# Optimization experiments

Hardware: AMD Instinct MI355X
Metric: run time of the kernel (lower is better)

Reference implementation:

```python
import jax, jax.numpy as jnp
import numpy as np

B, T, DIM = 2, 2048, 1024
HID = 4096
H, KVH, HD = 16, 4, 64
WIN = 512
NORM_EPS = 1e-5
QK_EPS = 1e-6
LS_INIT = 0.01


def setup_inputs() -> dict:
    key = jax.random.key(0)
    ks = jax.random.split(key, 12)
    s = lambda fan_in: 1.0 / np.sqrt(fan_in)
    return {
        "x": jax.random.normal(ks[0], (B, T, DIM), jnp.float32),
        # torch Linear weights are (out, in); y = x @ W.T
        "wq": jax.random.normal(ks[1], (H * HD, DIM), jnp.float32) * s(DIM),
        "wk": jax.random.normal(ks[2], (KVH * HD, DIM), jnp.float32) * s(DIM),
        "wv": jax.random.normal(ks[3], (KVH * HD, DIM), jnp.float32) * s(DIM),
        "wo": jax.random.normal(ks[4], (DIM, H * HD), jnp.float32) * s(H * HD),
        "w1": jax.random.normal(ks[5], (HID, DIM), jnp.float32) * s(DIM),
        "w2": jax.random.normal(ks[6], (DIM, HID), jnp.float32) * s(HID),
        "w3": jax.random.normal(ks[7], (HID, DIM), jnp.float32) * s(DIM),
        "q_norm_w": jnp.ones((HD,), jnp.float32),
        "k_norm_w": jnp.ones((HD,), jnp.float32),
        "attn_norm_w": jnp.ones((DIM,), jnp.float32),
        "ffn_norm_w": jnp.ones((DIM,), jnp.float32),
        "attn_scale": jnp.full((DIM,), LS_INIT, jnp.float32),
        "ffn_scale": jnp.full((DIM,), LS_INIT, jnp.float32),
    }


def _rmsnorm(x, w, eps):
    return x * jax.lax.rsqrt(jnp.mean(x * x, axis=-1, keepdims=True) + eps) * w


def _attention(x, wq, wk, wv, wo, q_norm_w, k_norm_w):
    b, t, _ = x.shape
    q = (x @ wq.T).reshape(b, t, H, HD)
    k = (x @ wk.T).reshape(b, t, KVH, HD)
    v = (x @ wv.T).reshape(b, t, KVH, HD)
    q = _rmsnorm(q, q_norm_w, QK_EPS)
    k = _rmsnorm(k, k_norm_w, QK_EPS)
    # GQA: repeat kv heads to H heads
    rep = H // KVH
    k = jnp.repeat(k, rep, axis=2)  # (b,t,H,HD)
    v = jnp.repeat(v, rep, axis=2)
    scale = 1.0 / np.sqrt(HD)
    scores = jnp.einsum("bqhd,bkhd->bhqk", q, k) * scale  # (b,H,t,t)
    row = jnp.arange(t)[:, None]
    col = jnp.arange(t)[None, :]
    mask = (row >= col) & (row - col < WIN)  # (t,t) bool
    scores = jnp.where(mask[None, None], scores, -jnp.inf)
    probs = jax.nn.softmax(scores, axis=-1)
    y = jnp.einsum("bhqk,bkhd->bqhd", probs, v).reshape(b, t, H * HD)
    return y @ wo.T


def reference(x, wq, wk, wv, wo, w1, w2, w3, q_norm_w, k_norm_w,
              attn_norm_w, ffn_norm_w, attn_scale, ffn_scale):
    r = _attention(_rmsnorm(x, attn_norm_w, NORM_EPS), wq, wk, wv, wo,
                   q_norm_w, k_norm_w)
    h = x + r * attn_scale
    hn = _rmsnorm(h, ffn_norm_w, NORM_EPS)
    ffn = (jax.nn.silu(hn @ w1.T) * (hn @ w3.T)) @ w2.T
    return h + ffn * ffn_scale
```

## Files before the change

### kernel.cpp

```cpp
#include <hip/hip_runtime.h>

typedef unsigned short u16;
typedef unsigned int u32;
typedef unsigned char u8;
typedef short bf16x8 __attribute__((ext_vector_type(8)));
typedef float f32x4 __attribute__((ext_vector_type(4)));
typedef float f32x16 __attribute__((ext_vector_type(16)));
typedef int i32x4 __attribute__((ext_vector_type(4)));
typedef int i32x8 __attribute__((ext_vector_type(8)));

#define AS1 __attribute__((address_space(1)))
#define AS3 __attribute__((address_space(3)))

#define B_ 2
#define T_ 2048
#define DIM_ 1024
#define HID_ 4096
#define H_ 16
#define KVH_ 4
#define HD_ 64
#define WIN_ 512

#define SCALE_A 0x7C7C7C7C
#define SCALE_B 0x79797979

__device__ __forceinline__ u16 f2bf(float f) {
    union { float f; u32 u; } v; v.f = f;
    u32 r = v.u + 0x7FFFu + ((v.u >> 16) & 1u);
    return (u16)(r >> 16);
}
__device__ __forceinline__ float bf2f(u32 u) {
    union { u32 u; float f; } v; v.u = u << 16;
    return v.f;
}
__device__ __forceinline__ float4 ld4bf(const u16* p) {
    uint2 u = *(const uint2*)p;
    float4 r;
    r.x = bf2f(u.x & 0xFFFFu); r.y = bf2f(u.x >> 16);
    r.z = bf2f(u.y & 0xFFFFu); r.w = bf2f(u.y >> 16);
    return r;
}
__device__ __forceinline__ void load_lds16(const void* g, void* l) {
    __builtin_amdgcn_global_load_lds((AS1 void*)(g), (AS3 void*)(l), 16, 0, 0);
}
#define WAITBAR(N) asm volatile("s_waitcnt vmcnt(" #N ")\n\ts_barrier" ::: "memory")

__global__ __launch_bounds__(256) void mega_cvt(const float* __restrict__ wq,
                                                const float* __restrict__ wk,
                                                const float* __restrict__ wv,
                                                const float* __restrict__ wo,
                                                const float* __restrict__ w1,
                                                const float* __restrict__ w3,
                                                const float* __restrict__ w2,
                                                u16* __restrict__ wqkv,
                                                u16* __restrict__ wo_b,
                                                u8* __restrict__ w13_8,
                                                u8* __restrict__ w2_8) {
    int i = blockIdx.x * 256 + threadIdx.x;
    if (i < 655360) {
        const float* s; uint2* dbase; size_t didx;
        if (i < 262144)      { s = wq + (size_t)i * 4; dbase = (uint2*)wqkv; didx = i; }
        else if (i < 327680) { int f = i - 262144; s = wk + (size_t)f * 4; dbase = (uint2*)wqkv; didx = 262144 + f; }
        else if (i < 393216) { int f = i - 327680; s = wv + (size_t)f * 4; dbase = (uint2*)wqkv; didx = 327680 + f; }
        else                 { int f = i - 393216; s = wo + (size_t)f * 4; dbase = (uint2*)wo_b; didx = f; }
        float4 v = *(const float4*)s;
        u32 lo = (u32)f2bf(v.x) | ((u32)f2bf(v.y) << 16);
        u32 hi = (u32)f2bf(v.z) | ((u32)f2bf(v.w) << 16);
        dbase[didx] = make_uint2(lo, hi);
    } else {
        const float* s; u32* dbase; size_t didx;
        if (i < 1703936)      { int f = i - 655360;  int c = f >> 8; int n = (c >> 5) * 64 + (c & 31);
                                s = w1 + (size_t)f * 4; dbase = (u32*)w13_8; didx = (size_t)n * 256 + (f & 255); }
        else if (i < 2752512) { int f = i - 1703936; int c = f >> 8; int n = (c >> 5) * 64 + 32 + (c & 31);
                                s = w3 + (size_t)f * 4; dbase = (u32*)w13_8; didx = (size_t)n * 256 + (f & 255); }
        else                  { int f = i - 2752512; s = w2 + (size_t)f * 4; dbase = (u32*)w2_8; didx = f; }
        float4 v = *(const float4*)s;
        int p = __builtin_amdgcn_cvt_pk_fp8_f32(v.x * 64.f, v.y * 64.f, 0, false);
        p = __builtin_amdgcn_cvt_pk_fp8_f32(v.z * 64.f, v.w * 64.f, p, true);
        dbase[didx] = (u32)p;
    }
}

__global__ __launch_bounds__(256) void rmsnorm_kernel(const float* __restrict__ x,
                                                      const float* __restrict__ w,
                                                      u16* __restrict__ out, float eps) {
    int row = blockIdx.x, tid = threadIdx.x;
    const float4 v = ((const float4*)(x + (size_t)row * DIM_))[tid];
    float ss = v.x * v.x + v.y * v.y + v.z * v.z + v.w * v.w;
#pragma unroll
    for (int m = 1; m < 64; m <<= 1) ss += __shfl_xor(ss, m);
    __shared__ float part[4];
    if ((tid & 63) == 0) part[tid >> 6] = ss;
    __syncthreads();
    float tot = part[0] + part[1] + part[2] + part[3];
    float r = rsqrtf(tot * (1.0f / DIM_) + eps);
    const float4 wv = ((const float4*)w)[tid];
    u32 lo = (u32)f2bf(v.x * r * wv.x) | ((u32)f2bf(v.y * r * wv.y) << 16);
    u32 hi = (u32)f2bf(v.z * r * wv.z) | ((u32)f2bf(v.w * r * wv.w) << 16);
    ((uint2*)(out + (size_t)row * DIM_))[tid] = make_uint2(lo, hi);
}

__global__ __launch_bounds__(256) void fuse_attn_kernel(const float* __restrict__ x,
                                                        const u16* __restrict__ p,
                                                        const float* __restrict__ ascale,
                                                        const float* __restrict__ fnw,
                                                        float* __restrict__ h,
                                                        u8* __restrict__ xn8) {
    int row = blockIdx.x, tid = threadIdx.x;
    const float4 xv = ((const float4*)(x + (size_t)row * DIM_))[tid];
    float4 a0 = ld4bf(p + (size_t)row * DIM_ + tid * 4);
    float4 a1 = ld4bf(p + 4194304 + (size_t)row * DIM_ + tid * 4);
    const float4 sc = ((const float4*)ascale)[tid];
    float4 hv;
    hv.x = xv.x + (a0.x + a1.x) * sc.x;
    hv.y = xv.y + (a0.y + a1.y) * sc.y;
    hv.z = xv.z + (a0.z + a1.z) * sc.z;
    hv.w = xv.w + (a0.w + a1.w) * sc.w;
    ((float4*)(h + (size_t)row * DIM_))[tid] = hv;
    float ss = hv.x * hv.x + hv.y * hv.y + hv.z * hv.z + hv.w * hv.w;
#pragma unroll
    for (int m = 1; m < 64; m <<= 1) ss += __shfl_xor(ss, m);
    __shared__ float part[4];
    if ((tid & 63) == 0) part[tid >> 6] = ss;
    __syncthreads();
    float tot = part[0] + part[1] + part[2] + part[3];
    float r = rsqrtf(tot * (1.0f / DIM_) + 1e-5f) * 8.0f;
    const float4 wv = ((const float4*)fnw)[tid];
    int pk = __builtin_amdgcn_cvt_pk_fp8_f32(hv.x * r * wv.x, hv.y * r * wv.y, 0, false);
    pk = __builtin_amdgcn_cvt_pk_fp8_f32(hv.z * r * wv.z, hv.w * r * wv.w, pk, true);
    ((u32*)xn8)[(size_t)row * 256 + tid] = (u32)pk;
}

__global__ __launch_bounds__(256) void fuse_ffn_kernel(const float* __restrict__ h,
                                                       const u16* __restrict__ p,
                                                       const float* __restrict__ fscale,
                                                       float* __restrict__ out) {
    int row = blockIdx.x, tid = threadIdx.x;
    const float4 hv = ((const float4*)(h + (size_t)row * DIM_))[tid];
    size_t off = (size_t)row * DIM_ + tid * 4;
    float4 a0 = ld4bf(p + off);
    float4 a1 = ld4bf(p + 4194304 + off);
    float4 a2 = ld4bf(p + 8388608 + off);
    float4 a3 = ld4bf(p + 12582912 + off);
    const float4 sc = ((const float4*)fscale)[tid];
    float4 o;
    o.x = hv.x + (a0.x + a1.x + a2.x + a3.x) * sc.x;
    o.y = hv.y + (a0.y + a1.y + a2.y + a3.y) * sc.y;
    o.z = hv.z + (a0.z + a1.z + a2.z + a3.z) * sc.z;
    o.w = hv.w + (a0.w + a1.w + a2.w + a3.w) * sc.w;
    ((float4*)(out + (size_t)row * DIM_))[tid] = o;
}

__global__ __launch_bounds__(256) void qkv_post_kernel(const u16* __restrict__ qkv,
                                                       const float* __restrict__ qw,
                                                       const float* __restrict__ kw,
                                                       u16* __restrict__ Qb,
                                                       u16* __restrict__ Kb,
                                                       u16* __restrict__ Vb) {
    int bt = blockIdx.x;
    int b = bt >> 11, t = bt & (T_ - 1);
    int wave = threadIdx.x >> 6, lane = threadIdx.x & 63;
    const u16* row0 = qkv + (size_t)bt * 1536;
    const u16* row1 = row0 + 6291456;
    float qwl = qw[lane], kwl = kw[lane];
#pragma unroll
    for (int i = 0; i < 4; i++) {
        int h = wave * 4 + i;
        float v = bf2f(row0[h * 64 + lane]) + bf2f(row1[h * 64 + lane]);
        float ss = v * v;
#pragma unroll
        for (int m = 1; m < 64; m <<= 1) ss += __shfl_xor(ss, m);
        float r = rsqrtf(ss * (1.0f / 64.0f) + 1e-6f);
        Qb[(((size_t)(b * H_ + h)) * T_ + t) * HD_ + lane] = f2bf(v * r * qwl);
    }
    {
        float v = bf2f(row0[1024 + wave * 64 + lane]) + bf2f(row1[1024 + wave * 64 + lane]);
        float ss = v * v;
#pragma unroll
        for (int m = 1; m < 64; m <<= 1) ss += __shfl_xor(ss, m);
        float r = rsqrtf(ss * (1.0f / 64.0f) + 1e-6f);
        Kb[(((size_t)(b * KVH_ + wave)) * T_ + t) * HD_ + lane] = f2bf(v * r * kwl);
        float vv = bf2f(row0[1280 + wave * 64 + lane]) + bf2f(row1[1280 + wave * 64 + lane]);
        Vb[(((size_t)(b * KVH_ + wave)) * T_ + t) * HD_ + lane] = f2bf(vv);
    }
}

__global__ __launch_bounds__(256) void vtrans_kernel(const u16* __restrict__ Vb,
                                                     u16* __restrict__ Vt) {
    const int bk = blockIdx.x >> 5;
    const int t0 = (blockIdx.x & 31) * 64;
    const int tid = threadIdx.x;
    __shared__ __align__(16) u16 tile[64][64];
    const u16* src = Vb + ((size_t)bk * T_ + t0) * HD_;
#pragma unroll
    for (int i = 0; i < 2; i++) {
        int g = tid + i * 256;
        int r = g >> 3, c8 = g & 7;
        *(bf16x8*)&tile[r][c8 * 8] = *(const bf16x8*)(src + (size_t)r * HD_ + c8 * 8);
    }
    __syncthreads();
    const int d = tid >> 2, ts = (tid & 3) * 16;
    u16 buf[16];
#pragma unroll
    for (int j = 0; j < 16; j++) buf[j] = tile[ts + j][d];
    u16* dst = Vt + (size_t)bk * HD_ * T_ + (size_t)d * T_ + t0 + ts;
    *(bf16x8*)(dst) = *(const bf16x8*)&buf[0];
    *(bf16x8*)(dst + 8) = *(const bf16x8*)&buf[8];
}

__global__ __launch_bounds__(512, 2) void flash_kernel(const u16* __restrict__ Qb,
                                                       const u16* __restrict__ Kb,
                                                       const u16* __restrict__ Vt,
                                                       u16* __restrict__ Ob) {
    const int b = blockIdx.z, kvh = blockIdx.y, qt = blockIdx.x;
    const int q0 = qt * 64;
    const int tid = threadIdx.x, wave = tid >> 6, lane = tid & 63;
    const int head = wave & 3, qhalf = wave >> 2;
    const int h = kvh * 4 + head;
    const int m = lane & 15, quad = lane >> 4;

    __shared__ __align__(16) u16 Ks[2][4096];
    __shared__ __align__(16) u16 Vs[2][4096];
    __shared__ __align__(16) u16 Ps[8][16 * 72];

    const u16* Qp = Qb + ((size_t)(b * H_ + h) * T_) * HD_;
    const u16* Kp = Kb + ((size_t)(b * KVH_ + kvh) * T_) * HD_;
    const u16* Vp = Vt + ((size_t)(b * KVH_ + kvh) * HD_) * T_;

    const int qbase = q0 + qhalf * 32;
    bf16x8 qa[2][2];
#pragma unroll
    for (int qs = 0; qs < 2; qs++) {
        const u16* qp = Qp + (size_t)(qbase + qs * 16 + m) * 64 + quad * 8;
        qa[qs][0] = *(const bf16x8*)(qp);
        qa[qs][1] = *(const bf16x8*)(qp + 32);
    }

    f32x4 o[2][4] = {};
    float mrun[2] = {-1e30f, -1e30f}, lrun[2] = {0.f, 0.f};

    const int kt0 = (q0 >= WIN_) ? ((q0 - (WIN_ - 1)) >> 6) : 0;
    const int kt1 = qt;

    const int srow = tid >> 3;
    const int schunk = (tid & 7) ^ (srow & 7);
    const u16* Ksrc = Kp + (size_t)srow * 64 + schunk * 8;
    const u16* Vsrc = Vp + (size_t)srow * T_ + schunk * 8;
    const int ldsOff = wave * 512;

    load_lds16(Ksrc + (size_t)kt0 * 4096, &Ks[0][ldsOff]);
    load_lds16(Vsrc + kt0 * 64, &Vs[0][ldsOff]);

    for (int kt = kt0; kt <= kt1; ++kt) {
        const int kbase = kt << 6;
        const int cur = (kt - kt0) & 1;
        if (kt < kt1) {
            load_lds16(Ksrc + (size_t)(kt + 1) * 4096, &Ks[cur ^ 1][ldsOff]);
            load_lds16(Vsrc + (kt + 1) * 64, &Vs[cur ^ 1][ldsOff]);
            WAITBAR(2);
        } else {
            WAITBAR(0);
        }
        bf16x8 kf[4][2], vb[4][2];
#pragma unroll
        for (int st = 0; st < 4; st++) {
            const int r64 = (st * 16 + m) * 64;
#pragma unroll
            for (int hf = 0; hf < 2; hf++) {
                const int c = (((hf << 2) + quad) ^ (m & 7)) * 8;
                kf[st][hf] = *(const bf16x8*)&Ks[cur][r64 + c];
                vb[st][hf] = *(const bf16x8*)&Vs[cur][r64 + c];
            }
        }
#pragma unroll
        for (int qs = 0; qs < 2; qs++) {
            const int qlo_s = qbase + qs * 16;
            if (kbase <= qlo_s + 15 && kbase >= qlo_s - 574) {
                f32x4 s4[4];
#pragma unroll
                for (int st = 0; st < 4; st++) {
                    f32x4 z = {0.f, 0.f, 0.f, 0.f};
                    z = __builtin_amdgcn_mfma_f32_16x16x32_bf16(kf[st][0], qa[qs][0], z, 0, 0, 0);
                    z = __builtin_amdgcn_mfma_f32_16x16x32_bf16(kf[st][1], qa[qs][1], z, 0, 0, 0);
                    s4[st] = z;
                }
                float v[16];
                const bool full = (kbase + 63 <= qlo_s) && (kbase >= qlo_s - 496);
                if (full) {
#pragma unroll
                    for (int i = 0; i < 16; i++) v[i] = s4[i >> 2][i & 3] * 0.125f;
                } else {
                    const int D = qlo_s + m - kbase - quad * 4;
#pragma unroll
                    for (int st = 0; st < 4; st++)
#pragma unroll
                        for (int r = 0; r < 4; r++) {
                            int diff = D - st * 16 - r;
                            v[st * 4 + r] = ((u32)diff < (u32)WIN_) ? s4[st][r] * 0.125f : -INFINITY;
                        }
                }
                float t0 = fmaxf(fmaxf(fmaxf(v[0], v[1]), fmaxf(v[2], v[3])),
                                 fmaxf(fmaxf(v[4], v[5]), fmaxf(v[6], v[7])));
                float t1 = fmaxf(fmaxf(fmaxf(v[8], v[9]), fmaxf(v[10], v[11])),
                                 fmaxf(fmaxf(v[12], v[13]), fmaxf(v[14], v[15])));
                float rmax = fmaxf(t0, t1);
                rmax = fmaxf(rmax, __shfl_xor(rmax, 16));
                rmax = fmaxf(rmax, __shfl_xor(rmax, 32));
                float mnew = fmaxf(mrun[qs], rmax);
                float alpha = __expf(mrun[qs] - mnew);
                float p[16];
#pragma unroll
                for (int i = 0; i < 16; i++) p[i] = __expf(v[i] - mnew);
                float u0 = ((p[0] + p[1]) + (p[2] + p[3])) + ((p[4] + p[5]) + (p[6] + p[7]));
                float u1 = ((p[8] + p[9]) + (p[10] + p[11])) + ((p[12] + p[13]) + (p[14] + p[15]));
                float psum = u0 + u1;
                psum += __shfl_xor(psum, 16);
                psum += __shfl_xor(psum, 32);
                lrun[qs] = lrun[qs] * alpha + psum;
                mrun[qs] = mnew;
#pragma unroll
                for (int d = 0; d < 4; d++) {
                    o[qs][d][0] *= alpha; o[qs][d][1] *= alpha;
                    o[qs][d][2] *= alpha; o[qs][d][3] *= alpha;
                }
#pragma unroll
                for (int st = 0; st < 4; st++) {
                    u32 lo = (u32)f2bf(p[st * 4 + 0]) | ((u32)f2bf(p[st * 4 + 1]) << 16);
                    u32 hi = (u32)f2bf(p[st * 4 + 2]) | ((u32)f2bf(p[st * 4 + 3]) << 16);
                    *(uint2*)&Ps[wave][m * 72 + st * 16 + quad * 4] = make_uint2(lo, hi);
                }
                bf16x8 pa0 = *(const bf16x8*)&Ps[wave][m * 72 + quad * 8];
                bf16x8 pa1 = *(const bf16x8*)&Ps[wave][m * 72 + 32 + quad * 8];
#pragma unroll
                for (int d = 0; d < 4; d++) {
                    o[qs][d] = __builtin_amdgcn_mfma_f32_16x16x32_bf16(vb[d][0], pa0, o[qs][d], 0, 0, 0);
                    o[qs][d] = __builtin_amdgcn_mfma_f32_16x16x32_bf16(vb[d][1], pa1, o[qs][d], 0, 0, 0);
                }
            }
        }
        asm volatile("s_barrier" ::: "memory");
    }
#pragma unroll
    for (int qs = 0; qs < 2; qs++) {
        float inv = 1.0f / lrun[qs];
        u16* ob = Ob + ((size_t)(b * T_ + qbase + qs * 16 + m)) * (H_ * HD_) + h * HD_;
#pragma unroll
        for (int d = 0; d < 4; d++) {
            u32 lo = (u32)f2bf(o[qs][d][0] * inv) | ((u32)f2bf(o[qs][d][1] * inv) << 16);
            u32 hi = (u32)f2bf(o[qs][d][2] * inv) | ((u32)f2bf(o[qs][d][3] * inv) << 16);
            *(uint2*)(ob + d * 16 + quad * 4) = make_uint2(lo, hi);
        }
    }
}

__global__ __launch_bounds__(256) void gemm_bt(const u16* __restrict__ A,
                                               const u16* __restrict__ Bt,
                                               u16* __restrict__ Cb,
                                               int M, int N, int K, int KS) {
    __shared__ __align__(16) u16 As[2][4096];
    __shared__ __align__(16) u16 Bs[2][4096];
    const int tid = threadIdx.x, wave = tid >> 6, lane = tid & 63;
    const int m = lane & 15, quad = lane >> 4;
    const int m0 = blockIdx.y * 128, n0 = blockIdx.x * 128;
    const int wm = (wave >> 1) * 64, wn = (wave & 1) * 64;
    const int kb = blockIdx.z * KS;
    const int nIter = KS >> 5;
    const int slot = wave * 2;
    const int flat0 = slot * 512 + lane * 8;
    const int row0_ = flat0 >> 5, col0 = flat0 & 31;
    const int flat1 = (slot + 1) * 512 + lane * 8;
    const int row1_ = flat1 >> 5, col1 = flat1 & 31;

    f32x4 acc[4][4] = {};

    load_lds16(A + (size_t)(m0 + row0_) * K + kb + col0, &As[0][slot * 512]);
    load_lds16(Bt + (size_t)(n0 + row0_) * K + kb + col0, &Bs[0][slot * 512]);
    load_lds16(A + (size_t)(m0 + row1_) * K + kb + col1, &As[0][(slot + 1) * 512]);
    load_lds16(Bt + (size_t)(n0 + row1_) * K + kb + col1, &Bs[0][(slot + 1) * 512]);

    for (int it = 0; it < nIter; ++it) {
        __syncthreads();
        const int cur = it & 1;
        if (it + 1 < nIter) {
            const int nb = 1 - cur;
            const int k0 = kb + (it + 1) * 32;
            load_lds16(A + (size_t)(m0 + row0_) * K + k0 + col0, &As[nb][slot * 512]);
            load_lds16(Bt + (size_t)(n0 + row0_) * K + k0 + col0, &Bs[nb][slot * 512]);
            load_lds16(A + (size_t)(m0 + row1_) * K + k0 + col1, &As[nb][(slot + 1) * 512]);
            load_lds16(Bt + (size_t)(n0 + row1_) * K + k0 + col1, &Bs[nb][(slot + 1) * 512]);
        }
        bf16x8 af[4], bfr[4];
#pragma unroll
        for (int i = 0; i < 4; i++) af[i] = *(const bf16x8*)&As[cur][(wm + i * 16 + m) * 32 + quad * 8];
#pragma unroll
        for (int j = 0; j < 4; j++) bfr[j] = *(const bf16x8*)&Bs[cur][(wn + j * 16 + m) * 32 + quad * 8];
#pragma unroll
        for (int i = 0; i < 4; i++)
#pragma unroll
            for (int j = 0; j < 4; j++)
                acc[i][j] = __builtin_amdgcn_mfma_f32_16x16x32_bf16(af[i], bfr[j], acc[i][j], 0, 0, 0);
    }

    u16* Cz = Cb + (size_t)blockIdx.z * M * N;
#pragma unroll
    for (int i = 0; i < 4; i++) {
        int rowb = m0 + wm + i * 16 + quad * 4;
#pragma unroll
        for (int j = 0; j < 4; j++) {
            int col = n0 + wn + j * 16 + m;
#pragma unroll
            for (int r = 0; r < 4; r++)
                Cz[(size_t)(rowb + r) * N + col] = f2bf(acc[i][j][r]);
        }
    }
}

#define MFMA8(a, b, c) __builtin_amdgcn_mfma_scale_f32_32x32x64_f8f6f4(a, b, c, 0, 0, 0, SCALE_A, 0, SCALE_B)
#define PHASE_MFMA(I0, I1)                           \
    __builtin_amdgcn_s_setprio(1);                   \
    acc[I0][0] = MFMA8(a0, bf0, acc[I0][0]);         \
    acc[I0][1] = MFMA8(a0, bf1, acc[I0][1]);         \
    acc[I1][0] = MFMA8(a1, bf0, acc[I1][0]);         \
    acc[I1][1] = MFMA8(a1, bf1, acc[I1][1]);         \
    __builtin_amdgcn_s_setprio(0);

template <int MODE>
__global__ __launch_bounds__(512) void gemm_fp8(const u8* __restrict__ A,
                                                const u8* __restrict__ Bt,
                                                u16* __restrict__ Cb,
                                                u8* __restrict__ C8,
                                                int M, int N, int K, int KS) {
    __shared__ __align__(16) u8 As[2][32768];
    __shared__ __align__(16) u8 Bs[2][32768];
    const int tid = threadIdx.x, wave = tid >> 6, lane = tid & 63;
    const int l31 = lane & 31, lh = lane >> 5;
    const int m0 = blockIdx.y * 256, n0 = blockIdx.x * 256;
    const int wm = (wave >> 2) * 128, wn = (wave & 3) * 64;
    const int kb = blockIdx.z * KS;
    const int KT = KS >> 7;

    const int srow = ((wave & 3) << 6) + lane;
    const u8* Asrc = A + (size_t)m0 * K + (size_t)srow * K;
    const u8* Bsrc = Bt + (size_t)n0 * K + (size_t)srow * K;
    const int wv2 = wave >> 2;
    const int ldsW = (wave & 3) << 10;

    auto STAGE = [&](const u8* src, int kk, int ks, u8* lds) {
#pragma unroll
        for (int q = 0; q < 2; q++) {
            const int ch = ks * 4 + wv2 + 2 * q;
            load_lds16(src + kk + ch * 16, lds + (ch << 12) + ldsW);
        }
    };
    auto FRAG = [&](const u8* t, int ks, int row) -> i32x8 {
        const int c0 = ks * 4 + (lh << 1);
        union { i32x4 h[2]; i32x8 v; } u;
        u.h[0] = *(const i32x4*)(t + ((c0 << 8) + row) * 16);
        u.h[1] = *(const i32x4*)(t + (((c0 + 1) << 8) + row) * 16);
        return u.v;
    };

    f32x16 acc[4][2] = {};

    STAGE(Asrc, kb, 0, As[0]);
    STAGE(Bsrc, kb, 0, Bs[0]);
    STAGE(Asrc, kb, 1, As[0]);
    STAGE(Bsrc, kb, 1, Bs[0]);

    for (int kt = 0; kt < KT - 1; ++kt) {
        const int cur = kt & 1, nb = cur ^ 1;
        const u8* Ac = As[cur];
        const u8* Bc = Bs[cur];
        const int kn = kb + (kt + 1) * 128;
        i32x8 bf0, bf1, a0, a1;
        STAGE(Asrc, kn, 0, As[nb]);
        WAITBAR(6);
        bf0 = FRAG(Bc, 0, wn + l31);
        bf1 = FRAG(Bc, 0, wn + 32 + l31);
        a0 = FRAG(Ac, 0, wm + l31);
        a1 = FRAG(Ac, 0, wm + 32 + l31);
        PHASE_MFMA(0, 1)
        STAGE(Bsrc, kn, 0, Bs[nb]);
        a0 = FRAG(Ac, 0, wm + 64 + l31);
        a1 = FRAG(Ac, 0, wm + 96 + l31);
        PHASE_MFMA(2, 3)
        STAGE(Asrc, kn, 1, As[nb]);
        WAITBAR(6);
        bf0 = FRAG(Bc, 1, wn + l31);
        bf1 = FRAG(Bc, 1, wn + 32 + l31);
        a0 = FRAG(Ac, 1, wm + l31);
        a1 = FRAG(Ac, 1, wm + 32 + l31);
        PHASE_MFMA(0, 1)
        STAGE(Bsrc, kn, 1, Bs[nb]);
        a0 = FRAG(Ac, 1, wm + 64 + l31);
        a1 = FRAG(Ac, 1, wm + 96 + l31);
        PHASE_MFMA(2, 3)
    }
    {
        const int cur = (KT - 1) & 1;
        const u8* Ac = As[cur];
        const u8* Bc = Bs[cur];
        i32x8 bf0, bf1, a0, a1;
        WAITBAR(4);
        bf0 = FRAG(Bc, 0, wn + l31);
        bf1 = FRAG(Bc, 0, wn + 32 + l31);
        a0 = FRAG(Ac, 0, wm + l31);
        a1 = FRAG(Ac, 0, wm + 32 + l31);
        PHASE_MFMA(0, 1)
        a0 = FRAG(Ac, 0, wm + 64 + l31);
        a1 = FRAG(Ac, 0, wm + 96 + l31);
        PHASE_MFMA(2, 3)
        WAITBAR(0);
        bf0 = FRAG(Bc, 1, wn + l31);
        bf1 = FRAG(Bc, 1, wn + 32 + l31);
        a0 = FRAG(Ac, 1, wm + l31);
        a1 = FRAG(Ac, 1, wm + 32 + l31);
        PHASE_MFMA(0, 1)
        a0 = FRAG(Ac, 1, wm + 64 + l31);
        a1 = FRAG(Ac, 1, wm + 96 + l31);
        PHASE_MFMA(2, 3)
    }

    if (MODE == 0) {
        u16* Cz = Cb + (size_t)blockIdx.z * M * N;
#pragma unroll
        for (int i = 0; i < 4; i++)
#pragma unroll
            for (int j = 0; j < 2; j++) {
                int col = n0 + wn + j * 32 + l31;
#pragma unroll
                for (int reg = 0; reg < 16; reg++) {
                    int row = m0 + wm + i * 32 + (reg & 3) + 8 * (reg >> 2) + 4 * lh;
                    Cz[(size_t)row * N + col] = f2bf(acc[i][j][reg]);
                }
            }
    } else {
        int c = (n0 >> 1) + (wn >> 1) + l31;
#pragma unroll
        for (int i = 0; i < 4; i++)
#pragma unroll
            for (int reg = 0; reg < 16; reg++) {
                int row = m0 + wm + i * 32 + (reg & 3) + 8 * (reg >> 2) + 4 * lh;
                float g1 = acc[i][0][reg], g3 = acc[i][1][reg];
                float res = (g1 / (1.f + __expf(-g1))) * g3 * 8.0f;
                int p = __builtin_amdgcn_cvt_pk_fp8_f32(res, res, 0, false);
                C8[(size_t)row * (N >> 1) + c] = (u8)(p & 0xFF);
            }
    }
}

extern "C" void kernel_launch(void* const* d_in, const int* in_sizes, int n_in,
                              void* d_out, int out_size, void* d_ws, size_t ws_size,
                              hipStream_t stream) {
    const float* x = (const float*)d_in[0];
    const float* wq = (const float*)d_in[1];
    const float* wk = (const float*)d_in[2];
    const float* wv = (const float*)d_in[3];
    const float* wo = (const float*)d_in[4];
    const float* w1 = (const float*)d_in[5];
    const float* w2 = (const float*)d_in[6];
    const float* w3 = (const float*)d_in[7];
    const float* qnw = (const float*)d_in[8];
    const float* knw = (const float*)d_in[9];
    const float* anw = (const float*)d_in[10];
    const float* fnw = (const float*)d_in[11];
    const float* ascale = (const float*)d_in[12];
    const float* fscale = (const float*)d_in[13];
    float* out = (float*)d_out;

    char* ws = (char*)d_ws;
    u16* wqkv_bf = (u16*)(ws + 0);
    u16* wo_bf = (u16*)(ws + 3145728);
    u8* w13_8 = (u8*)(ws + 5242880);
    u8* w2_8 = (u8*)(ws + 13631488);
    u16* xn_bf = (u16*)(ws + 17825792);
    u8* xn8 = (u8*)(ws + 26214400);
    float* h_f = (float*)(ws + 30408704);
    char* P = ws + 47185920;
    u16* qkv_part = (u16*)(P + 0);
    u16* Qb = (u16*)(P + 25165824);
    u16* Kb = (u16*)(P + 33554432);
    u16* Vb = (u16*)(P + 35651584);
    u16* att_bf = (u16*)(P + 37748736);
    u16* Vt = (u16*)(P + 46137344);
    u16* wo_part = (u16*)(P + 0);
    u8* gsw8 = (u8*)(P + 16777216);
    u16* w2_part = (u16*)(P + 33554432);

    mega_cvt<<<14848, 256, 0, stream>>>(wq, wk, wv, wo, w1, w3, w2,
                                        wqkv_bf, wo_bf, w13_8, w2_8);
    rmsnorm_kernel<<<4096, 256, 0, stream>>>(x, anw, xn_bf, 1e-5f);
    gemm_bt<<<dim3(12, 32, 2), 256, 0, stream>>>(xn_bf, wqkv_bf, qkv_part,
                                                 4096, 1536, 1024, 512);
    qkv_post_kernel<<<4096, 256, 0, stream>>>(qkv_part, qnw, knw, Qb, Kb, Vb);
    vtrans_kernel<<<256, 256, 0, stream>>>(Vb, Vt);
    flash_kernel<<<dim3(32, KVH_, B_), 512, 0, stream>>>(Qb, Kb, Vt, att_bf);
    gemm_bt<<<dim3(8, 32, 2), 256, 0, stream>>>(att_bf, wo_bf, wo_part,
                                                4096, 1024, 1024, 512);
    fuse_attn_kernel<<<4096, 256, 0, stream>>>(x, wo_part, ascale, fnw, h_f, xn8);
    gemm_fp8<1><<<dim3(32, 16, 1), 512, 0, stream>>>(xn8, w13_8, nullptr, gsw8,
                                                     4096, 8192, 1024, 1024);
    gemm_fp8<0><<<dim3(4, 16, 4), 512, 0, stream>>>(gsw8, w2_8, w2_part, nullptr,
                                                    4096, 1024, 4096, 1024);
    fuse_ffn_kernel<<<4096, 256, 0, stream>>>(h_f, w2_part, fscale, out);
}
```

Measured before the change: 319.7 us.

## Switch FP8 GEMM to 128x128 tiles with 16x16x128 scaled MFMA

Replaces the 256x256-tile, 512-thread FP8 GEMM used for the FFN projections with a 128x128-tile, 256-thread version. It uses 16x16x128 scaled MFMA instructions and a simple double-buffered loop with one barrier per k-step. Smaller tiles and less LDS per block aim to raise occupancy and grid size. In exchange it loses the hand-interleaved staging, priority hints and per-tile data reuse of the larger tile.

Result: slower. 352.6 us (+10.3%).

```diff
diff --git a/kernel.cpp b/kernel.cpp
--- a/kernel.cpp
+++ b/kernel.cpp
@@ -415,137 +415,96 @@
     }
 }
 
-#define MFMA8(a, b, c) __builtin_amdgcn_mfma_scale_f32_32x32x64_f8f6f4(a, b, c, 0, 0, 0, SCALE_A, 0, SCALE_B)
-#define PHASE_MFMA(I0, I1)                           \
-    __builtin_amdgcn_s_setprio(1);                   \
-    acc[I0][0] = MFMA8(a0, bf0, acc[I0][0]);         \
-    acc[I0][1] = MFMA8(a0, bf1, acc[I0][1]);         \
-    acc[I1][0] = MFMA8(a1, bf0, acc[I1][0]);         \
-    acc[I1][1] = MFMA8(a1, bf1, acc[I1][1]);         \
-    __builtin_amdgcn_s_setprio(0);
+#define MFMA16(a, b, c) __builtin_amdgcn_mfma_scale_f32_16x16x128_f8f6f4(a, b, c, 0, 0, 0, SCALE_A, 0, SCALE_B)
 
 template <int MODE>
-__global__ __launch_bounds__(512) void gemm_fp8(const u8* __restrict__ A,
+__global__ __launch_bounds__(256) void gemm_fp8(const u8* __restrict__ A,
                                                 const u8* __restrict__ Bt,
                                                 u16* __restrict__ Cb,
                                                 u8* __restrict__ C8,
                                                 int M, int N, int K, int KS) {
-    __shared__ __align__(16) u8 As[2][32768];
-    __shared__ __align__(16) u8 Bs[2][32768];
+    __shared__ __align__(16) u8 As[2][16384];
+    __shared__ __align__(16) u8 Bs[2][16384];
     const int tid = threadIdx.x, wave = tid >> 6, lane = tid & 63;
-    const int l31 = lane & 31, lh = lane >> 5;
-    const int m0 = blockIdx.y * 256, n0 = blockIdx.x * 256;
-    const int wm = (wave >> 2) * 128, wn = (wave & 3) * 64;
+    const int m = lane & 15, quad = lane >> 4;
+    const int m0 = blockIdx.y * 128, n0 = blockIdx.x * 128;
+    const int wm = (wave >> 1) * 64, wn = (wave & 1) * 64;
     const int kb = blockIdx.z * KS;
-    const int KT = KS >> 7;
-
-    const int srow = ((wave & 3) << 6) + lane;
-    const u8* Asrc = A + (size_t)m0 * K + (size_t)srow * K;
-    const u8* Bsrc = Bt + (size_t)n0 * K + (size_t)srow * K;
-    const int wv2 = wave >> 2;
-    const int ldsW = (wave & 3) << 10;
-
-    auto STAGE = [&](const u8* src, int kk, int ks, u8* lds) {
-#pragma unroll
-        for (int q = 0; q < 2; q++) {
-            const int ch = ks * 4 + wv2 + 2 * q;
-            load_lds16(src + kk + ch * 16, lds + (ch << 12) + ldsW);
+    const int nIter = KS >> 7;
+
+    const u8* Ab = A + (size_t)m0 * K;
+    const u8* Bb = Bt + (size_t)n0 * K;
+
+    auto STAGE = [&](const u8* src, int kk, u8* lds) {
+#pragma unroll
+        for (int s = 0; s < 4; s++) {
+            const int g = wave * 64 + lane + s * 256;
+            const int r = g & 127, c = g >> 7;
+            load_lds16(src + (size_t)r * K + kk + c * 16,
+                       lds + (size_t)(wave * 64 + s * 256) * 16);
         }
     };
-    auto FRAG = [&](const u8* t, int ks, int row) -> i32x8 {
-        const int c0 = ks * 4 + (lh << 1);
+    auto FRAG = [&](const u8* t, int row) -> i32x8 {
         union { i32x4 h[2]; i32x8 v; } u;
-        u.h[0] = *(const i32x4*)(t + ((c0 << 8) + row) * 16);
-        u.h[1] = *(const i32x4*)(t + (((c0 + 1) << 8) + row) * 16);
+        u.h[0] = *(const i32x4*)(t + (((quad * 2 + 0) << 7) + row) * 16);
+        u.h[1] = *(const i32x4*)(t + (((quad * 2 + 1) << 7) + row) * 16);
         return u.v;
     };
 
-    f32x16 acc[4][2] = {};
-
-    STAGE(Asrc, kb, 0, As[0]);
-    STAGE(Bsrc, kb, 0, Bs[0]);
-    STAGE(Asrc, kb, 1, As[0]);
-    STAGE(Bsrc, kb, 1, Bs[0]);
-
-    for (int kt = 0; kt < KT - 1; ++kt) {
-        const int cur = kt & 1, nb = cur ^ 1;
-        const u8* Ac = As[cur];
-        const u8* Bc = Bs[cur];
-        const int kn = kb + (kt + 1) * 128;
-        i32x8 bf0, bf1, a0, a1;
-        STAGE(Asrc, kn, 0, As[nb]);
-        WAITBAR(6);
-        bf0 = FRAG(Bc, 0, wn + l31);
-        bf1 = FRAG(Bc, 0, wn + 32 + l31);
-        a0 = FRAG(Ac, 0, wm + l31);
-        a1 = FRAG(Ac, 0, wm + 32 + l31);
-        PHASE_MFMA(0, 1)
-        STAGE(Bsrc, kn, 0, Bs[nb]);
-        a0 = FRAG(Ac, 0, wm + 64 + l31);
-        a1 = FRAG(Ac, 0, wm + 96 + l31);
-        PHASE_MFMA(2, 3)
-        STAGE(Asrc, kn, 1, As[nb]);
-        WAITBAR(6);
-        bf0 = FRAG(Bc, 1, wn + l31);
-        bf1 = FRAG(Bc, 1, wn + 32 + l31);
-        a0 = FRAG(Ac, 1, wm + l31);
-        a1 = FRAG(Ac, 1, wm + 32 + l31);
-        PHASE_MFMA(0, 1)
-        STAGE(Bsrc, kn, 1, Bs[nb]);
-        a0 = FRAG(Ac, 1, wm + 64 + l31);
-        a1 = FRAG(Ac, 1, wm + 96 + l31);
-        PHASE_MFMA(2, 3)
-    }
-    {
-        const int cur = (KT - 1) & 1;
-        const u8* Ac = As[cur];
-        const u8* Bc = Bs[cur];
-        i32x8 bf0, bf1, a0, a1;
-        WAITBAR(4);
-        bf0 = FRAG(Bc, 0, wn + l31);
-        bf1 = FRAG(Bc, 0, wn + 32 + l31);
-        a0 = FRAG(Ac, 0, wm + l31);
-        a1 = FRAG(Ac, 0, wm + 32 + l31);
-        PHASE_MFMA(0, 1)
-        a0 = FRAG(Ac, 0, wm + 64 + l31);
-        a1 = FRAG(Ac, 0, wm + 96 + l31);
-        PHASE_MFMA(2, 3)
-        WAITBAR(0);
-        bf0 = FRAG(Bc, 1, wn + l31);
-        bf1 = FRAG(Bc, 1, wn + 32 + l31);
-        a0 = FRAG(Ac, 1, wm + l31);
-        a1 = FRAG(Ac, 1, wm + 32 + l31);
-        PHASE_MFMA(0, 1)
-        a0 = FRAG(Ac, 1, wm + 64 + l31);
-        a1 = FRAG(Ac, 1, wm + 96 + l31);
-        PHASE_MFMA(2, 3)
+    f32x4 acc[4][4] = {};
+
+    STAGE(Ab, kb, As[0]);
+    STAGE(Bb, kb, Bs[0]);
+
+    for (int it = 0; it < nIter; ++it) {
+        __syncthreads();
+        const int cur = it & 1;
+        if (it + 1 < nIter) {
+            STAGE(Ab, kb + (it + 1) * 128, As[1 - cur]);
+            STAGE(Bb, kb + (it + 1) * 128, Bs[1 - cur]);
+        }
+        i32x8 af[4], bfr[4];
+#pragma unroll
+        for (int i = 0; i < 4; i++) af[i] = FRAG(As[cur], wm + i * 16 + m);
+#pragma unroll
+        for (int j = 0; j < 4; j++) bfr[j] = FRAG(Bs[cur], wn + j * 16 + m);
+#pragma unroll
+        for (int i = 0; i < 4; i++)
+#pragma unroll
+            for (int j = 0; j < 4; j++)
+                acc[i][j] = MFMA16(af[i], bfr[j], acc[i][j]);
     }
 
     if (MODE == 0) {
         u16* Cz = Cb + (size_t)blockIdx.z * M * N;
 #pragma unroll
-        for (int i = 0; i < 4; i++)
-#pragma unroll
-            for (int j = 0; j < 2; j++) {
-                int col = n0 + wn + j * 32 + l31;
-#pragma unroll
-                for (int reg = 0; reg < 16; reg++) {
-                    int row = m0 + wm + i * 32 + (reg & 3) + 8 * (reg >> 2) + 4 * lh;
-                    Cz[(size_t)row * N + col] = f2bf(acc[i][j][reg]);
+        for (int i = 0; i < 4; i++) {
+            int rowb = m0 + wm + i * 16 + quad * 4;
+#pragma unroll
+            for (int j = 0; j < 4; j++) {
+                int col = n0 + wn + j * 16 + m;
+#pragma unroll
+                for (int r = 0; r < 4; r++)
+                    Cz[(size_t)(rowb + r) * N + col] = f2bf(acc[i][j][r]);
+            }
+        }
+    } else {
+        const int cbase = (n0 + wn) >> 1;
+#pragma unroll
+        for (int i = 0; i < 4; i++) {
+            int rowb = m0 + wm + i * 16 + quad * 4;
+#pragma unroll
+            for (int jj = 0; jj < 2; jj++) {
+                int c = cbase + jj * 16 + m;
+#pragma unroll
+                for (int r = 0; r < 4; r++) {
+                    float g1 = acc[i][jj][r], g3 = acc[i][jj + 2][r];
+                    float res = (g1 / (1.f + __expf(-g1))) * g3 * 8.0f;
+                    int p = __builtin_amdgcn_cvt_pk_fp8_f32(res, res, 0, false);
+                    C8[(size_t)(rowb + r) * (N >> 1) + c] = (u8)(p & 0xFF);
                 }
             }
-    } else {
-        int c = (n0 >> 1) + (wn >> 1) + l31;
-#pragma unroll
-        for (int i = 0; i < 4; i++)
-#pragma unroll
-            for (int reg = 0; reg < 16; reg++) {
-                int row = m0 + wm + i * 32 + (reg & 3) + 8 * (reg >> 2) + 4 * lh;
-                float g1 = acc[i][0][reg], g3 = acc[i][1][reg];
-                float res = (g1 / (1.f + __expf(-g1))) * g3 * 8.0f;
-                int p = __builtin_amdgcn_cvt_pk_fp8_f32(res, res, 0, false);
-                C8[(size_t)row * (N >> 1) + c] = (u8)(p & 0xFF);
-            }
+        }
     }
 }
 
@@ -598,9 +557,9 @@
     gemm_bt<<<dim3(8, 32, 2), 256, 0, stream>>>(att_bf, wo_bf, wo_part,
                                                 4096, 1024, 1024, 512);
     fuse_attn_kernel<<<4096, 256, 0, stream>>>(x, wo_part, ascale, fnw, h_f, xn8);
-    gemm_fp8<1><<<dim3(32, 16, 1), 512, 0, stream>>>(xn8, w13_8, nullptr, gsw8,
+    gemm_fp8<1><<<dim3(64, 32, 1), 256, 0, stream>>>(xn8, w13_8, nullptr, gsw8,
                                                      4096, 8192, 1024, 1024);
-    gemm_fp8<0><<<dim3(4, 16, 4), 512, 0, stream>>>(gsw8, w2_8, w2_part, nullptr,
+    gemm_fp8<0><<<dim3(8, 32, 4), 256, 0, stream>>>(gsw8, w2_8, w2_part, nullptr,
                                                     4096, 1024, 4096, 1024);
     fuse_ffn_kernel<<<4096, 256, 0, stream>>>(h_f, w2_part, fscale, out);
 }
```

## Switch fp8 GEMM LDS tiles to row-major XOR-swizzled layout with simpler pipeline

Applied to the files above, without the earlier changes.

Changes the shared-memory tile layout of the fp8 GEMM from column-chunk-major to row-major with an XOR swizzle on 16-byte chunks, so global loads read contiguous row segments and LDS fragment reads avoid bank conflicts. The fine-grained interleaving of staging and MFMA phases is replaced by a simpler loop. Each iteration issues the whole next tile's loads after a barrier, waits, then runs both k-substeps. This trades the previous finer overlap of loads with compute for coalesced global access and conflict-free LDS reads.

Result: faster. 306.2 us (-4.2%).

```diff
diff --git a/kernel.cpp b/kernel.cpp
--- a/kernel.cpp
+++ b/kernel.cpp
@@ -439,86 +439,62 @@
     const int kb = blockIdx.z * KS;
     const int KT = KS >> 7;
 
-    const int srow = ((wave & 3) << 6) + lane;
-    const u8* Asrc = A + (size_t)m0 * K + (size_t)srow * K;
-    const u8* Bsrc = Bt + (size_t)n0 * K + (size_t)srow * K;
-    const int wv2 = wave >> 2;
-    const int ldsW = (wave & 3) << 10;
-
-    auto STAGE = [&](const u8* src, int kk, int ks, u8* lds) {
-#pragma unroll
-        for (int q = 0; q < 2; q++) {
-            const int ch = ks * 4 + wv2 + 2 * q;
-            load_lds16(src + kk + ch * 16, lds + (ch << 12) + ldsW);
+    const u8* Ab = A + (size_t)m0 * K;
+    const u8* Bb = Bt + (size_t)n0 * K;
+
+    auto STAGE = [&](const u8* src, int kk, int h, u8* lds) {
+#pragma unroll
+        for (int p = 0; p < 2; p++) {
+            const int s = p * 512 + tid;
+            const int r = (h << 7) + (s >> 3);
+            const int c = (s & 7) ^ (r & 7);
+            load_lds16(src + (size_t)r * K + kk + c * 16,
+                       lds + (h << 14) + (p << 13) + (wave << 10));
         }
     };
     auto FRAG = [&](const u8* t, int ks, int row) -> i32x8 {
         const int c0 = ks * 4 + (lh << 1);
+        const u8* rp = t + row * 128;
         union { i32x4 h[2]; i32x8 v; } u;
-        u.h[0] = *(const i32x4*)(t + ((c0 << 8) + row) * 16);
-        u.h[1] = *(const i32x4*)(t + (((c0 + 1) << 8) + row) * 16);
+        u.h[0] = *(const i32x4*)(rp + ((c0 ^ (row & 7)) << 4));
+        u.h[1] = *(const i32x4*)(rp + (((c0 + 1) ^ (row & 7)) << 4));
         return u.v;
     };
 
     f32x16 acc[4][2] = {};
 
-    STAGE(Asrc, kb, 0, As[0]);
-    STAGE(Bsrc, kb, 0, Bs[0]);
-    STAGE(Asrc, kb, 1, As[0]);
-    STAGE(Bsrc, kb, 1, Bs[0]);
-
-    for (int kt = 0; kt < KT - 1; ++kt) {
-        const int cur = kt & 1, nb = cur ^ 1;
-        const u8* Ac = As[cur];
-        const u8* Bc = Bs[cur];
-        const int kn = kb + (kt + 1) * 128;
-        i32x8 bf0, bf1, a0, a1;
-        STAGE(Asrc, kn, 0, As[nb]);
-        WAITBAR(6);
-        bf0 = FRAG(Bc, 0, wn + l31);
-        bf1 = FRAG(Bc, 0, wn + 32 + l31);
-        a0 = FRAG(Ac, 0, wm + l31);
-        a1 = FRAG(Ac, 0, wm + 32 + l31);
-        PHASE_MFMA(0, 1)
-        STAGE(Bsrc, kn, 0, Bs[nb]);
-        a0 = FRAG(Ac, 0, wm + 64 + l31);
-        a1 = FRAG(Ac, 0, wm + 96 + l31);
-        PHASE_MFMA(2, 3)
-        STAGE(Asrc, kn, 1, As[nb]);
-        WAITBAR(6);
-        bf0 = FRAG(Bc, 1, wn + l31);
-        bf1 = FRAG(Bc, 1, wn + 32 + l31);
-        a0 = FRAG(Ac, 1, wm + l31);
-        a1 = FRAG(Ac, 1, wm + 32 + l31);
-        PHASE_MFMA(0, 1)
-        STAGE(Bsrc, kn, 1, Bs[nb]);
-        a0 = FRAG(Ac, 1, wm + 64 + l31);
-        a1 = FRAG(Ac, 1, wm + 96 + l31);
-        PHASE_MFMA(2, 3)
-    }
-    {
-        const int cur = (KT - 1) & 1;
+    STAGE(Ab, kb, 0, As[0]);
+    STAGE(Ab, kb, 1, As[0]);
+    STAGE(Bb, kb, 0, Bs[0]);
+    STAGE(Bb, kb, 1, Bs[0]);
+
+    for (int kt = 0; kt < KT; ++kt) {
+        const int cur = kt & 1;
+        if (kt + 1 < KT) {
+            asm volatile("s_barrier" ::: "memory");
+            const int kn = kb + (kt + 1) * 128;
+            STAGE(Ab, kn, 0, As[1 - cur]);
+            STAGE(Ab, kn, 1, As[1 - cur]);
+            STAGE(Bb, kn, 0, Bs[1 - cur]);
+            STAGE(Bb, kn, 1, Bs[1 - cur]);
+            WAITBAR(8);
+        } else {
+            WAITBAR(0);
+        }
         const u8* Ac = As[cur];
         const u8* Bc = Bs[cur];
         i32x8 bf0, bf1, a0, a1;
-        WAITBAR(4);
-        bf0 = FRAG(Bc, 0, wn + l31);
-        bf1 = FRAG(Bc, 0, wn + 32 + l31);
-        a0 = FRAG(Ac, 0, wm + l31);
-        a1 = FRAG(Ac, 0, wm + 32 + l31);
-        PHASE_MFMA(0, 1)
-        a0 = FRAG(Ac, 0, wm + 64 + l31);
-        a1 = FRAG(Ac, 0, wm + 96 + l31);
-        PHASE_MFMA(2, 3)
-        WAITBAR(0);
-        bf0 = FRAG(Bc, 1, wn + l31);
-        bf1 = FRAG(Bc, 1, wn + 32 + l31);
-        a0 = FRAG(Ac, 1, wm + l31);
-        a1 = FRAG(Ac, 1, wm + 32 + l31);
-        PHASE_MFMA(0, 1)
-        a0 = FRAG(Ac, 1, wm + 64 + l31);
-        a1 = FRAG(Ac, 1, wm + 96 + l31);
-        PHASE_MFMA(2, 3)
+#pragma unroll
+        for (int ks = 0; ks < 2; ks++) {
+            bf0 = FRAG(Bc, ks, wn + l31);
+            bf1 = FRAG(Bc, ks, wn + 32 + l31);
+            a0 = FRAG(Ac, ks, wm + l31);
+            a1 = FRAG(Ac, ks, wm + 32 + l31);
+            PHASE_MFMA(0, 1)
+            a0 = FRAG(Ac, ks, wm + 64 + l31);
+            a1 = FRAG(Ac, ks, wm + 96 + l31);
+            PHASE_MFMA(2, 3)
+        }
     }
 
     if (MODE == 0) {
```
